# Kernel tuning notes

Measured on AMD Instinct MI355X. Metric: run time of the kernel, lower is better.

Reference implementation:

```python
import jax, jax.numpy as jnp
import numpy as np

N_BINS = 15


def setup_inputs() -> dict:
    key = jax.random.key(0)
    k1, k2 = jax.random.split(key)
    logits = jax.random.normal(k1, (1000000, 256), dtype=jnp.float32)
    labels = jax.random.randint(k2, (1000000,), 0, 256, dtype=jnp.int64)
    return {"logits": logits, "labels": labels}


def reference(logits, labels):
    # softmax -> per-sample confidence (max prob) and prediction (argmax)
    probs = jax.nn.softmax(logits, axis=-1)
    confidences = jnp.max(probs, axis=-1)            # [N]
    predictions = jnp.argmax(probs, axis=-1)         # [N]
    accuracies = (predictions == labels).astype(logits.dtype)

    # Bin i covers (i/n_bins, (i+1)/n_bins]: searchsorted(side='left') - 1.
    boundaries = jnp.linspace(0.0, 1.0, N_BINS + 1, dtype=logits.dtype)
    bin_idx = jnp.clip(jnp.searchsorted(boundaries, confidences, side="left") - 1, 0, N_BINS - 1)

    n = confidences.shape[0]
    counts = jax.ops.segment_sum(jnp.ones_like(confidences), bin_idx, num_segments=N_BINS)
    conf_sum = jax.ops.segment_sum(confidences, bin_idx, num_segments=N_BINS)
    acc_sum = jax.ops.segment_sum(accuracies, bin_idx, num_segments=N_BINS)

    safe_counts = jnp.maximum(counts, 1.0)
    gap = jnp.abs(conf_sum / safe_counts - acc_sum / safe_counts)   # |avg_conf - acc| per bin
    ece = jnp.sum(jnp.where(counts > 0, gap * counts / n, 0.0))
    return ece.reshape(1)
```

## Files before the change

### kernel.cpp

```cpp
#include <hip/hip_runtime.h>

#define N_BINS 15
#define NSTATS (3 * N_BINS)
#define NBLK   2048
#define ROWS   4

template <int CTRL>
__device__ __forceinline__ float dpp_fmax(float x) {
    int xi = __float_as_int(x);
    int mv = __builtin_amdgcn_update_dpp(xi, xi, CTRL, 0xF, 0xF, true);
    return fmaxf(x, __int_as_float(mv));
}
template <int CTRL>
__device__ __forceinline__ float dpp_fadd(float x) {
    int xi = __float_as_int(x);
    int mv = __builtin_amdgcn_update_dpp(xi, xi, CTRL, 0xF, 0xF, true);
    return x + __int_as_float(mv);
}


__global__ __launch_bounds__(256) void ece_main_p(const float* __restrict__ logits,
                                                  const int* __restrict__ labels,
                                                  float* __restrict__ partials,
                                                  int n_rows) {
    __shared__ float sbins[NSTATS];
    for (int i = threadIdx.x; i < NSTATS; i += 256) sbins[i] = 0.0f;
    __syncthreads();

    const int lane = threadIdx.x & 63;
    const int g    = lane >> 4;
    const int t    = lane & 15;
    const int wv   = threadIdx.x >> 6;
    const int gwave = blockIdx.x * 4 + wv;
    const int step  = NBLK * 4 * ROWS;

    for (int base = gwave * ROWS; base < n_rows; base += step) {
        const int  r     = base + g;
        const bool valid = (r < n_rows);

        float4 v0, v1, v2, v3;
        float  lab_logit = 0.0f;
        if (valid) {
            const unsigned off4 = ((unsigned)r << 6) + ((unsigned)t << 2);
            const float4* p = reinterpret_cast<const float4*>(logits) + off4;
            v0 = p[0]; v1 = p[1]; v2 = p[2]; v3 = p[3];
            const int lab = labels[r];
            lab_logit = logits[((unsigned)r << 8) + (unsigned)lab];
        } else {
            v0 = v1 = v2 = v3 = make_float4(-1e30f, -1e30f, -1e30f, -1e30f);
        }

        float m = fmaxf(fmaxf(fmaxf(v0.x, v0.y), fmaxf(v0.z, v0.w)),
                        fmaxf(fmaxf(v1.x, v1.y), fmaxf(v1.z, v1.w)));
        m = fmaxf(m, fmaxf(fmaxf(fmaxf(v2.x, v2.y), fmaxf(v2.z, v2.w)),
                           fmaxf(fmaxf(v3.x, v3.y), fmaxf(v3.z, v3.w))));

        float s = ((__expf(v0.x) + __expf(v0.y)) + (__expf(v0.z) + __expf(v0.w)))
                + ((__expf(v1.x) + __expf(v1.y)) + (__expf(v1.z) + __expf(v1.w)))
                + ((__expf(v2.x) + __expf(v2.y)) + (__expf(v2.z) + __expf(v2.w)))
                + ((__expf(v3.x) + __expf(v3.y)) + (__expf(v3.z) + __expf(v3.w)));

        m = dpp_fmax<0x128>(m);  s = dpp_fadd<0x128>(s);
        m = dpp_fmax<0x124>(m);  s = dpp_fadd<0x124>(s);
        m = dpp_fmax<0x4E>(m);   s = dpp_fadd<0x4E>(s);
        m = dpp_fmax<0xB1>(m);   s = dpp_fadd<0xB1>(s);

        if (t == 0 && valid) {
            const float conf = __expf(m) / s;
            const float acc  = (lab_logit == m) ? 1.0f : 0.0f;

            int bin = (int)ceilf(conf * 15.0f) - 1;
            bin = bin < 0 ? 0 : (bin > N_BINS - 1 ? N_BINS - 1 : bin);

            atomicAdd(&sbins[bin], 1.0f);
            atomicAdd(&sbins[N_BINS + bin], conf);
            atomicAdd(&sbins[2 * N_BINS + bin], acc);
        }
    }

    __syncthreads();
    for (int i = threadIdx.x; i < NSTATS; i += 256)
        partials[i * NBLK + blockIdx.x] = sbins[i];
}

__global__ __launch_bounds__(1024) void ece_final_p(const float* __restrict__ partials,
                                                    float* __restrict__ out, float n) {
    __shared__ float stat[NSTATS];
    const int wv   = threadIdx.x >> 6;
    const int lane = threadIdx.x & 63;
    for (int s = wv; s < NSTATS; s += 16) {
        float acc = 0.0f;
        #pragma unroll 4
        for (int b = lane; b < NBLK; b += 64) acc += partials[s * NBLK + b];
        #pragma unroll
        for (int off = 32; off >= 1; off >>= 1) acc += __shfl_xor(acc, off);
        if (lane == 0) stat[s] = acc;
    }
    __syncthreads();
    if (threadIdx.x == 0) {
        float ece = 0.0f;
        for (int i = 0; i < N_BINS; ++i) {
            const float c = stat[i];
            if (c > 0.0f) {
                const float sc  = c < 1.0f ? 1.0f : c;
                const float gap = fabsf(stat[N_BINS + i] / sc - stat[2 * N_BINS + i] / sc);
                ece += gap * c / n;
            }
        }
        out[0] = ece;
    }
}


__global__ void ece_zero_ws(float* __restrict__ ws) {
    int i = threadIdx.x;
    if (i < NSTATS) ws[i] = 0.0f;
}

__global__ __launch_bounds__(256) void ece_main_a(const float* __restrict__ logits,
                                                  const int* __restrict__ labels,
                                                  float* __restrict__ ws,
                                                  int n_rows) {
    __shared__ float sbins[NSTATS];
    for (int i = threadIdx.x; i < NSTATS; i += 256) sbins[i] = 0.0f;
    __syncthreads();

    const int lane = threadIdx.x & 63;
    const int g = lane >> 4, t = lane & 15;
    const int wv = threadIdx.x >> 6;
    const int gwave = blockIdx.x * 4 + wv;
    const int step  = NBLK * 4 * ROWS;

    for (int base = gwave * ROWS; base < n_rows; base += step) {
        const int  r     = base + g;
        const bool valid = (r < n_rows);
        float4 v0, v1, v2, v3;
        float lab_logit = 0.0f;
        if (valid) {
            const unsigned off4 = ((unsigned)r << 6) + ((unsigned)t << 2);
            const float4* p = reinterpret_cast<const float4*>(logits) + off4;
            v0 = p[0]; v1 = p[1]; v2 = p[2]; v3 = p[3];
            const int lab = labels[r];
            lab_logit = logits[((unsigned)r << 8) + (unsigned)lab];
        } else {
            v0 = v1 = v2 = v3 = make_float4(-1e30f, -1e30f, -1e30f, -1e30f);
        }
        float m = fmaxf(fmaxf(fmaxf(v0.x, v0.y), fmaxf(v0.z, v0.w)),
                        fmaxf(fmaxf(v1.x, v1.y), fmaxf(v1.z, v1.w)));
        m = fmaxf(m, fmaxf(fmaxf(fmaxf(v2.x, v2.y), fmaxf(v2.z, v2.w)),
                           fmaxf(fmaxf(v3.x, v3.y), fmaxf(v3.z, v3.w))));
        float s = ((__expf(v0.x) + __expf(v0.y)) + (__expf(v0.z) + __expf(v0.w)))
                + ((__expf(v1.x) + __expf(v1.y)) + (__expf(v1.z) + __expf(v1.w)))
                + ((__expf(v2.x) + __expf(v2.y)) + (__expf(v2.z) + __expf(v2.w)))
                + ((__expf(v3.x) + __expf(v3.y)) + (__expf(v3.z) + __expf(v3.w)));
        m = dpp_fmax<0x128>(m);  s = dpp_fadd<0x128>(s);
        m = dpp_fmax<0x124>(m);  s = dpp_fadd<0x124>(s);
        m = dpp_fmax<0x4E>(m);   s = dpp_fadd<0x4E>(s);
        m = dpp_fmax<0xB1>(m);   s = dpp_fadd<0xB1>(s);
        if (t == 0 && valid) {
            const float conf = __expf(m) / s;
            const float acc  = (lab_logit == m) ? 1.0f : 0.0f;
            int bin = (int)ceilf(conf * 15.0f) - 1;
            bin = bin < 0 ? 0 : (bin > N_BINS - 1 ? N_BINS - 1 : bin);
            atomicAdd(&sbins[bin], 1.0f);
            atomicAdd(&sbins[N_BINS + bin], conf);
            atomicAdd(&sbins[2 * N_BINS + bin], acc);
        }
    }
    __syncthreads();
    for (int i = threadIdx.x; i < NSTATS; i += 256) {
        const float val = sbins[i];
        if (val != 0.0f) atomicAdd(&ws[i], val);
    }
}

__global__ void ece_final_a(const float* __restrict__ ws, float* __restrict__ out, float n) {
    float ece = 0.0f;
    for (int i = 0; i < N_BINS; ++i) {
        const float c = ws[i];
        if (c > 0.0f) {
            const float sc  = c < 1.0f ? 1.0f : c;
            const float gap = fabsf(ws[N_BINS + i] / sc - ws[2 * N_BINS + i] / sc);
            ece += gap * c / n;
        }
    }
    out[0] = ece;
}


extern "C" void kernel_launch(void* const* d_in, const int* in_sizes, int n_in,
                              void* d_out, int out_size, void* d_ws, size_t ws_size,
                              hipStream_t stream) {
    const float* logits = (const float*)d_in[0];
    const int*   labels = (const int*)d_in[1];
    float* out = (float*)d_out;
    float* ws  = (float*)d_ws;
    const int n_rows = in_sizes[1];

    const size_t needed = (size_t)NSTATS * NBLK * sizeof(float);
    if (ws_size >= needed) {
        ece_main_p<<<NBLK, 256, 0, stream>>>(logits, labels, ws, n_rows);
        ece_final_p<<<1, 1024, 0, stream>>>(ws, out, (float)n_rows);
    } else {
        ece_zero_ws<<<1, 64, 0, stream>>>(ws);
        ece_main_a<<<NBLK, 256, 0, stream>>>(logits, labels, ws, n_rows);
        ece_final_a<<<1, 1, 0, stream>>>(ws, out, (float)n_rows);
    }
}
```

Baseline: 187.5 us.

## Map each row across a full wavefront and take label logit from registers

Instead of 16 lanes per row with each lane loading four strided float4s, each wavefront now processes four rows with all 64 lanes loading one contiguous float4 per row. Reductions become full 64-lane DPP, swizzle and shuffle chains, and the label logit is selected from registers by the owning lane rather than re-read with a scattered global load. This aims for fully coalesced loads and removes the extra per-row random access, at the cost of four separate wave-wide reductions per iteration, each including an LDS-based cross-row step.

```diff
diff --git a/kernel.cpp b/kernel.cpp
--- a/kernel.cpp
+++ b/kernel.cpp
@@ -16,6 +16,35 @@
     int xi = __float_as_int(x);
     int mv = __builtin_amdgcn_update_dpp(xi, xi, CTRL, 0xF, 0xF, true);
     return x + __int_as_float(mv);
+}
+
+__device__ __forceinline__ float red64_fmax(float x) {
+    x = dpp_fmax<0x128>(x);
+    x = dpp_fmax<0x124>(x);
+    x = dpp_fmax<0x4E>(x);
+    x = dpp_fmax<0xB1>(x);
+    x = fmaxf(x, __int_as_float(__builtin_amdgcn_ds_swizzle(__float_as_int(x), 0x401F)));
+    x = fmaxf(x, __shfl_xor(x, 32));
+    return x;
+}
+__device__ __forceinline__ float red64_fadd(float x) {
+    x = dpp_fadd<0x128>(x);
+    x = dpp_fadd<0x124>(x);
+    x = dpp_fadd<0x4E>(x);
+    x = dpp_fadd<0xB1>(x);
+    x += __int_as_float(__builtin_amdgcn_ds_swizzle(__float_as_int(x), 0x401F));
+    x += __shfl_xor(x, 32);
+    return x;
+}
+
+__device__ __forceinline__ float local_max4(float4 v) {
+    return fmaxf(fmaxf(v.x, v.y), fmaxf(v.z, v.w));
+}
+__device__ __forceinline__ float local_expsum4(float4 v) {
+    return (__expf(v.x) + __expf(v.y)) + (__expf(v.z) + __expf(v.w));
+}
+__device__ __forceinline__ float sel4(float4 v, int c) {
+    return (c & 1) ? ((c & 2) ? v.w : v.y) : ((c & 2) ? v.z : v.x);
 }
 
 
@@ -27,55 +56,55 @@
     for (int i = threadIdx.x; i < NSTATS; i += 256) sbins[i] = 0.0f;
     __syncthreads();
 
-    const int lane = threadIdx.x & 63;
-    const int g    = lane >> 4;
-    const int t    = lane & 15;
-    const int wv   = threadIdx.x >> 6;
+    const int lane  = threadIdx.x & 63;
+    const int wv    = threadIdx.x >> 6;
     const int gwave = blockIdx.x * 4 + wv;
     const int step  = NBLK * 4 * ROWS;
 
     for (int base = gwave * ROWS; base < n_rows; base += step) {
-        const int  r     = base + g;
-        const bool valid = (r < n_rows);
-
+        const float4* p = reinterpret_cast<const float4*>(logits) + (unsigned)base * 64u + (unsigned)lane;
         float4 v0, v1, v2, v3;
-        float  lab_logit = 0.0f;
-        if (valid) {
-            const unsigned off4 = ((unsigned)r << 6) + ((unsigned)t << 2);
-            const float4* p = reinterpret_cast<const float4*>(logits) + off4;
-            v0 = p[0]; v1 = p[1]; v2 = p[2]; v3 = p[3];
-            const int lab = labels[r];
-            lab_logit = logits[((unsigned)r << 8) + (unsigned)lab];
+        int lab0 = 0, lab1 = 0, lab2 = 0, lab3 = 0;
+        const bool full = (base + ROWS <= n_rows);
+        if (full) {
+            v0 = p[0]; v1 = p[64]; v2 = p[128]; v3 = p[192];
+            lab0 = labels[base]; lab1 = labels[base + 1];
+            lab2 = labels[base + 2]; lab3 = labels[base + 3];
         } else {
-            v0 = v1 = v2 = v3 = make_float4(-1e30f, -1e30f, -1e30f, -1e30f);
-        }
-
-        float m = fmaxf(fmaxf(fmaxf(v0.x, v0.y), fmaxf(v0.z, v0.w)),
-                        fmaxf(fmaxf(v1.x, v1.y), fmaxf(v1.z, v1.w)));
-        m = fmaxf(m, fmaxf(fmaxf(fmaxf(v2.x, v2.y), fmaxf(v2.z, v2.w)),
-                           fmaxf(fmaxf(v3.x, v3.y), fmaxf(v3.z, v3.w))));
-
-        float s = ((__expf(v0.x) + __expf(v0.y)) + (__expf(v0.z) + __expf(v0.w)))
-                + ((__expf(v1.x) + __expf(v1.y)) + (__expf(v1.z) + __expf(v1.w)))
-                + ((__expf(v2.x) + __expf(v2.y)) + (__expf(v2.z) + __expf(v2.w)))
-                + ((__expf(v3.x) + __expf(v3.y)) + (__expf(v3.z) + __expf(v3.w)));
-
-        m = dpp_fmax<0x128>(m);  s = dpp_fadd<0x128>(s);
-        m = dpp_fmax<0x124>(m);  s = dpp_fadd<0x124>(s);
-        m = dpp_fmax<0x4E>(m);   s = dpp_fadd<0x4E>(s);
-        m = dpp_fmax<0xB1>(m);   s = dpp_fadd<0xB1>(s);
-
-        if (t == 0 && valid) {
-            const float conf = __expf(m) / s;
-            const float acc  = (lab_logit == m) ? 1.0f : 0.0f;
-
-            int bin = (int)ceilf(conf * 15.0f) - 1;
-            bin = bin < 0 ? 0 : (bin > N_BINS - 1 ? N_BINS - 1 : bin);
-
-            atomicAdd(&sbins[bin], 1.0f);
-            atomicAdd(&sbins[N_BINS + bin], conf);
-            atomicAdd(&sbins[2 * N_BINS + bin], acc);
-        }
+            const float4 neg = make_float4(-1e30f, -1e30f, -1e30f, -1e30f);
+            v0 = (base + 0 < n_rows) ? p[0]   : neg;
+            v1 = (base + 1 < n_rows) ? p[64]  : neg;
+            v2 = (base + 2 < n_rows) ? p[128] : neg;
+            v3 = (base + 3 < n_rows) ? p[192] : neg;
+            if (base + 0 < n_rows) lab0 = labels[base + 0];
+            if (base + 1 < n_rows) lab1 = labels[base + 1];
+            if (base + 2 < n_rows) lab2 = labels[base + 2];
+            if (base + 3 < n_rows) lab3 = labels[base + 3];
+        }
+
+        float m0 = local_max4(v0), m1 = local_max4(v1), m2 = local_max4(v2), m3 = local_max4(v3);
+        float s0 = local_expsum4(v0), s1 = local_expsum4(v1), s2 = local_expsum4(v2), s3 = local_expsum4(v3);
+
+        const float e0 = sel4(v0, lab0 & 3), e1 = sel4(v1, lab1 & 3);
+        const float e2 = sel4(v2, lab2 & 3), e3 = sel4(v3, lab3 & 3);
+        const bool o0 = ((lab0 >> 2) == lane), o1 = ((lab1 >> 2) == lane);
+        const bool o2 = ((lab2 >> 2) == lane), o3 = ((lab3 >> 2) == lane);
+
+        m0 = red64_fmax(m0); m1 = red64_fmax(m1); m2 = red64_fmax(m2); m3 = red64_fmax(m3);
+        s0 = red64_fadd(s0); s1 = red64_fadd(s1); s2 = red64_fadd(s2); s3 = red64_fadd(s3);
+
+        #define ECE_EMIT(J)                                                         \
+        if (o##J && (base + J < n_rows)) {                                          \
+            const float conf = __expf(m##J) / s##J;                                 \
+            const float acc  = (e##J == m##J) ? 1.0f : 0.0f;                        \
+            int bin = (int)ceilf(conf * 15.0f) - 1;                                 \
+            bin = bin < 0 ? 0 : (bin > N_BINS - 1 ? N_BINS - 1 : bin);              \
+            atomicAdd(&sbins[bin], 1.0f);                                           \
+            atomicAdd(&sbins[N_BINS + bin], conf);                                  \
+            atomicAdd(&sbins[2 * N_BINS + bin], acc);                               \
+        }
+        ECE_EMIT(0) ECE_EMIT(1) ECE_EMIT(2) ECE_EMIT(3)
+        #undef ECE_EMIT
     }
 
     __syncthreads();
@@ -125,47 +154,53 @@
     for (int i = threadIdx.x; i < NSTATS; i += 256) sbins[i] = 0.0f;
     __syncthreads();
 
-    const int lane = threadIdx.x & 63;
-    const int g = lane >> 4, t = lane & 15;
-    const int wv = threadIdx.x >> 6;
+    const int lane  = threadIdx.x & 63;
+    const int wv    = threadIdx.x >> 6;
     const int gwave = blockIdx.x * 4 + wv;
     const int step  = NBLK * 4 * ROWS;
 
     for (int base = gwave * ROWS; base < n_rows; base += step) {
-        const int  r     = base + g;
-        const bool valid = (r < n_rows);
+        const float4* p = reinterpret_cast<const float4*>(logits) + (unsigned)base * 64u + (unsigned)lane;
         float4 v0, v1, v2, v3;
-        float lab_logit = 0.0f;
-        if (valid) {
-            const unsigned off4 = ((unsigned)r << 6) + ((unsigned)t << 2);
-            const float4* p = reinterpret_cast<const float4*>(logits) + off4;
-            v0 = p[0]; v1 = p[1]; v2 = p[2]; v3 = p[3];
-            const int lab = labels[r];
-            lab_logit = logits[((unsigned)r << 8) + (unsigned)lab];
+        int lab0 = 0, lab1 = 0, lab2 = 0, lab3 = 0;
+        const bool full = (base + ROWS <= n_rows);
+        if (full) {
+            v0 = p[0]; v1 = p[64]; v2 = p[128]; v3 = p[192];
+            lab0 = labels[base]; lab1 = labels[base + 1];
+            lab2 = labels[base + 2]; lab3 = labels[base + 3];
         } else {
-            v0 = v1 = v2 = v3 = make_float4(-1e30f, -1e30f, -1e30f, -1e30f);
-        }
-        float m = fmaxf(fmaxf(fmaxf(v0.x, v0.y), fmaxf(v0.z, v0.w)),
-                        fmaxf(fmaxf(v1.x, v1.y), fmaxf(v1.z, v1.w)));
-        m = fmaxf(m, fmaxf(fmaxf(fmaxf(v2.x, v2.y), fmaxf(v2.z, v2.w)),
-                           fmaxf(fmaxf(v3.x, v3.y), fmaxf(v3.z, v3.w))));
-        float s = ((__expf(v0.x) + __expf(v0.y)) + (__expf(v0.z) + __expf(v0.w)))
-                + ((__expf(v1.x) + __expf(v1.y)) + (__expf(v1.z) + __expf(v1.w)))
-                + ((__expf(v2.x) + __expf(v2.y)) + (__expf(v2.z) + __expf(v2.w)))
-                + ((__expf(v3.x) + __expf(v3.y)) + (__expf(v3.z) + __expf(v3.w)));
-        m = dpp_fmax<0x128>(m);  s = dpp_fadd<0x128>(s);
-        m = dpp_fmax<0x124>(m);  s = dpp_fadd<0x124>(s);
-        m = dpp_fmax<0x4E>(m);   s = dpp_fadd<0x4E>(s);
-        m = dpp_fmax<0xB1>(m);   s = dpp_fadd<0xB1>(s);
-        if (t == 0 && valid) {
-            const float conf = __expf(m) / s;
-            const float acc  = (lab_logit == m) ? 1.0f : 0.0f;
-            int bin = (int)ceilf(conf * 15.0f) - 1;
-            bin = bin < 0 ? 0 : (bin > N_BINS - 1 ? N_BINS - 1 : bin);
-            atomicAdd(&sbins[bin], 1.0f);
-            atomicAdd(&sbins[N_BINS + bin], conf);
-            atomicAdd(&sbins[2 * N_BINS + bin], acc);
-        }
+            const float4 neg = make_float4(-1e30f, -1e30f, -1e30f, -1e30f);
+            v0 = (base + 0 < n_rows) ? p[0]   : neg;
+            v1 = (base + 1 < n_rows) ? p[64]  : neg;
+            v2 = (base + 2 < n_rows) ? p[128] : neg;
+            v3 = (base + 3 < n_rows) ? p[192] : neg;
+            if (base + 0 < n_rows) lab0 = labels[base + 0];
+            if (base + 1 < n_rows) lab1 = labels[base + 1];
+            if (base + 2 < n_rows) lab2 = labels[base + 2];
+            if (base + 3 < n_rows) lab3 = labels[base + 3];
+        }
+
+        float m0 = local_max4(v0), m1 = local_max4(v1), m2 = local_max4(v2), m3 = local_max4(v3);
+        float s0 = local_expsum4(v0), s1 = local_expsum4(v1), s2 = local_expsum4(v2), s3 = local_expsum4(v3);
+        const float e0 = sel4(v0, lab0 & 3), e1 = sel4(v1, lab1 & 3);
+        const float e2 = sel4(v2, lab2 & 3), e3 = sel4(v3, lab3 & 3);
+        const bool o0 = ((lab0 >> 2) == lane), o1 = ((lab1 >> 2) == lane);
+        const bool o2 = ((lab2 >> 2) == lane), o3 = ((lab3 >> 2) == lane);
+        m0 = red64_fmax(m0); m1 = red64_fmax(m1); m2 = red64_fmax(m2); m3 = red64_fmax(m3);
+        s0 = red64_fadd(s0); s1 = red64_fadd(s1); s2 = red64_fadd(s2); s3 = red64_fadd(s3);
+
+        #define ECE_EMIT(J)                                                         \
+        if (o##J && (base + J < n_rows)) {                                          \
+            const float conf = __expf(m##J) / s##J;                                 \
+            const float acc  = (e##J == m##J) ? 1.0f : 0.0f;                        \
+            int bin = (int)ceilf(conf * 15.0f) - 1;                                 \
+            bin = bin < 0 ? 0 : (bin > N_BINS - 1 ? N_BINS - 1 : bin);              \
+            atomicAdd(&sbins[bin], 1.0f);                                           \
+            atomicAdd(&sbins[N_BINS + bin], conf);                                  \
+            atomicAdd(&sbins[2 * N_BINS + bin], acc);                               \
+        }
+        ECE_EMIT(0) ECE_EMIT(1) ECE_EMIT(2) ECE_EMIT(3)
+        #undef ECE_EMIT
     }
     __syncthreads();
     for (int i = threadIdx.x; i < NSTATS; i += 256) {
```

Measured after the change: 198.4 us. 5.8% more time.
